# Kernel tuning notes

Measured on AMD Instinct MI355X. Metric: run time of the kernel, lower is better.

## Reference

```python
import jax, jax.numpy as jnp
import numpy as np

N_PHI = 64
NK = 16
NS = 8
B = 512
BN_EPS = 1e-3  # keras BatchNormalization default
LRELU_ALPHA = 0.1


def _cplx(re, im):
    return jax.lax.complex(re, im)


def _conjT(x):
    return jnp.conj(jnp.swapaxes(x, -1, -2))


def setup_inputs() -> dict:
    key = jax.random.key(0)
    ks = jax.random.split(key, 10)

    def cn(k, shape, scale=1.0):
        kr, ki = jax.random.split(k)
        return scale * _cplx(jax.random.normal(kr, shape, jnp.float32),
                             jax.random.normal(ki, shape, jnp.float32))

    # Phi: unit-modulus RIS phase matrix [B, 64, 64]
    theta = jax.random.uniform(ks[0], (B, N_PHI, N_PHI), jnp.float32, 0.0, 2.0 * np.pi)
    Phi = _cplx(jnp.cos(theta), jnp.sin(theta))

    # G_hat_k^H : [Nk, B, 64, Ns]
    G_h = cn(ks[1], (NK, B, N_PHI, NS), 1.0 / np.sqrt(N_PHI))

    # Lam_k: Hermitian PSD + I -> invertible, [Nk, B, Ns, Ns]
    A = cn(ks[2], (NK, B, NS, NS), 0.3)
    Lam = A @ _conjT(A) + jnp.eye(NS, dtype=jnp.complex64)

    # C_k: Hermitian PSD + eps*I, [Nk, B, 64, 64]
    D = cn(ks[3], (NK, B, N_PHI, N_PHI), 0.1)
    C = D @ _conjT(D) + 0.1 * jnp.eye(N_PHI, dtype=jnp.complex64)

    Beta = jax.random.uniform(ks[4], (NK, B, 1, 1), jnp.float32, 0.5, 1.5)

    return {
        "Phi_re": jnp.real(Phi), "Phi_im": jnp.imag(Phi),
        "G_h_re": jnp.real(G_h), "G_h_im": jnp.imag(G_h),
        "Lam_re": jnp.real(Lam), "Lam_im": jnp.imag(Lam),
        "C_re": jnp.real(C), "C_im": jnp.imag(C),
        "Beta": Beta,
        "bn_gamma": jnp.ones((2 * N_PHI,), jnp.float32),
        "bn_beta": jnp.zeros((2 * N_PHI,), jnp.float32),
        "bn_mean": 0.1 * jax.random.normal(ks[5], (2 * N_PHI,), jnp.float32),
        "bn_var": jax.random.uniform(ks[6], (2 * N_PHI,), jnp.float32, 0.5, 1.5),
        "w": 0.1 * jax.random.normal(ks[7], (2 * N_PHI, 1), jnp.float32),
        "b": jnp.zeros((1,), jnp.float32),
    }


def _forward(Phi_re, Phi_im, G_h_re, G_h_im, Lam_re, Lam_im, C_re, C_im, Beta,
             bn_gamma, bn_beta, bn_mean, bn_var, w, b):
    Phi = _cplx(Phi_re, Phi_im)            # [B, 64, 64]
    G_h = _cplx(G_h_re, G_h_im)            # [Nk, B, 64, Ns]
    Lam = _cplx(Lam_re, Lam_im)            # [Nk, B, Ns, Ns]
    C = _cplx(C_re, C_im)                  # [Nk, B, 64, 64]
    Beta_c = _cplx(Beta, jnp.zeros_like(Beta))

    # --- learned step size: Phi @ ones(64,1) == row sums -> BN -> Dense(leaky_relu) ---
    Phi_p_vec = jnp.sum(Phi, axis=2)                                   # [B, 64]
    iq = jnp.concatenate([jnp.real(Phi_p_vec), jnp.imag(Phi_p_vec)], axis=1)  # [B, 128]
    t = bn_gamma * (iq - bn_mean) * jax.lax.rsqrt(bn_var + BN_EPS) + bn_beta
    s = t @ w + b                                                      # [B, 1]
    step = jnp.where(s >= 0, s, LRELU_ALPHA * s)

    # --- batched per-user Euclidean gradient (replaces python loop over Nk) ---
    G = _conjT(G_h)                                                    # [Nk, B, Ns, 64]
    M = jnp.einsum('kbse,bef->kbsf', G, Phi)                           # G_k @ Phi
    T = jnp.einsum('kbsf,kbfg->kbsg', M, C)                            # G_k Phi C_k
    Q = jnp.linalg.inv(Lam) + T @ _conjT(M) / Beta_c                   # [Nk, B, Ns, Ns]
    Qi = jnp.linalg.inv(Q)
    Qi2 = Qi @ Qi
    eg_k = jnp.einsum('kbfs,kbst,kbtg->kbfg', G_h, Qi2, T) / Beta_c    # [Nk, B, 64, 64]
    eg = -(jnp.sum(eg_k, axis=0) / NK) * jnp.eye(N_PHI, dtype=jnp.complex64)

    # --- Riemannian gradient / projection step ---
    proj = jnp.real(eg * jnp.conj(Phi))
    rg = eg - _cplx(proj, jnp.zeros_like(proj)) * Phi
    nrm = jnp.sqrt(jnp.sum(jnp.abs(rg) ** 2, axis=(1, 2), keepdims=True))  # fro norm [B,1,1]
    nrm_c = _cplx(nrm, jnp.zeros_like(nrm))
    step_c = _cplx(step, jnp.zeros_like(step))[:, :, None]             # [B, 1, 1]
    Phi_new = Phi - step_c * rg / nrm_c

    # --- magnitude constraint |Phi| <= 1 ---
    ab = jnp.abs(Phi_new)
    den = jnp.maximum(ab - 1.0, 0.0) + 1.0
    return Phi_new / _cplx(den, jnp.zeros_like(den))


def reference(Phi_re, Phi_im, G_h_re, G_h_im, Lam_re, Lam_im, C_re, C_im, Beta,
              bn_gamma, bn_beta, bn_mean, bn_var, w, b):
    return _forward(Phi_re, Phi_im, G_h_re, G_h_im, Lam_re, Lam_im, C_re, C_im,
                    Beta, bn_gamma, bn_beta, bn_mean, bn_var, w, b)
```

## Files before the change

### kernel.cpp

```cpp
#include <hip/hip_runtime.h>

#define NPHI 64
#define NS 8
#define NK 16
#define BATCH 512

typedef __attribute__((__ext_vector_type__(2))) float v2f;

#define PK_BL(acc, p, b)  asm("v_pk_fma_f32 %0, %1, %2, %0 op_sel:[0,0,0] op_sel_hi:[1,0,1]" : "+v"(acc) : "v"(p), "v"(b))
#define PK_BH(acc, p, b)  asm("v_pk_fma_f32 %0, %1, %2, %0 op_sel:[0,1,0] op_sel_hi:[1,1,1]" : "+v"(acc) : "v"(p), "v"(b))
#define PK_BLN(acc, p, b) asm("v_pk_fma_f32 %0, %1, %2, %0 op_sel:[0,0,0] op_sel_hi:[1,0,1] neg_lo:[0,1,0] neg_hi:[0,1,0]" : "+v"(acc) : "v"(p), "v"(b))
#define PK_X(acc, p, b)   asm("v_pk_fma_f32 %0, %1, %2, %0 op_sel:[1,1,0] op_sel_hi:[0,1,1] neg_lo:[1,0,0]" : "+v"(acc) : "v"(p), "v"(b))
#define PK_XH(acc, p, b)  asm("v_pk_fma_f32 %0, %1, %2, %0 op_sel:[1,1,0] op_sel_hi:[0,1,1] neg_hi:[1,0,0]" : "+v"(acc) : "v"(p), "v"(b))
#define PK_XLO(acc, p, b) asm("v_pk_fma_f32 %0, %1, %2, %0 op_sel:[1,0,0] op_sel_hi:[0,0,1] neg_hi:[1,0,0]" : "+v"(acc) : "v"(p), "v"(b))

__device__ __forceinline__ void cinv8(float& ar, float& ai, int lane) {
    const int i = lane >> 3, j = lane & 7;
#pragma unroll
    for (int p = 0; p < 8; ++p) {
        const float pr = __shfl(ar, p * 9, 64);
        const float pi = __shfl(ai, p * 9, 64);
        const float den = pr * pr + pi * pi;
        const float rr = pr / den, ri = -pi / den;
        const float aipr = __shfl(ar, (i << 3) | p, 64);
        const float aipi = __shfl(ai, (i << 3) | p, 64);
        const float apjr = __shfl(ar, (p << 3) | j, 64);
        const float apji = __shfl(ai, (p << 3) | j, 64);
        const float br = rr * apjr - ri * apji;
        const float bi = rr * apji + ri * apjr;
        const float er = ar - (aipr * br - aipi * bi);
        const float ei = ai - (aipr * bi + aipi * br);
        const float rowr = rr * ar - ri * ai;
        const float rowi = rr * ai + ri * ar;
        const bool ip = (i == p), jp = (j == p);
        const float nr = ip ? (jp ? rr : rowr) : (jp ? -rowr : er);
        const float ni = ip ? (jp ? ri : rowi) : (jp ? -rowi : ei);
        ar = nr; ai = ni;
    }
}

__global__ __launch_bounds__(256, 2) void k_grad_diag(
    const float* __restrict__ PhiR, const float* __restrict__ PhiI,
    const float* __restrict__ GhR, const float* __restrict__ GhI,
    const float* __restrict__ LamR, const float* __restrict__ LamI,
    const float* __restrict__ CR, const float* __restrict__ CI,
    const float* __restrict__ Beta,
    float* __restrict__ out, int region)
{
    const int tid = threadIdx.x;
    const int w = tid >> 6;
    const int lane = tid & 63;
    const int gw = blockIdx.x * 4 + w;
    const int k = gw & (NK - 1);
    const int b = gw >> 4;
    const int kb = k * BATCH + b;

    __shared__ __align__(16) float2 sM[4][NPHI][10];
    __shared__ float2 sQ2[4][64];

    const float* phiR = PhiR + b * 4096;
    const float* phiI = PhiI + b * 4096;
    const float* ghR = GhR + kb * 512;
    const float* ghI = GhI + kb * 512;
    const float invb = 1.0f / Beta[kb];

    v2f accr[4], acci[4];
    v2f acc2[8];

    {
#pragma unroll
        for (int sp = 0; sp < 4; ++sp) { accr[sp] = (v2f)0.f; acci[sp] = (v2f)0.f; }
        float pA[4], qA[4], pB[4], qB[4];
#pragma unroll
        for (int u = 0; u < 4; ++u) {
            pA[u] = phiR[u * 64 + lane];
            qA[u] = phiI[u * 64 + lane];
        }
#pragma unroll 1
        for (int eb = 0; eb < 64; eb += 8) {
#pragma unroll
            for (int u = 0; u < 4; ++u) {
                pB[u] = phiR[(eb + 4 + u) * 64 + lane];
                qB[u] = phiI[(eb + 4 + u) * 64 + lane];
            }
#pragma unroll
            for (int u = 0; u < 4; ++u) {
                const int e = eb + u;
                const v2f* g2 = (const v2f*)(ghR + e * 8);
                const v2f* h2 = (const v2f*)(ghI + e * 8);
                v2f pp; pp.x = pA[u]; pp.y = qA[u];
#pragma unroll
                for (int sp = 0; sp < 4; ++sp) {
                    const v2f g = g2[sp];
                    const v2f h = h2[sp];
                    PK_BL(accr[sp], g, pp);
                    PK_BH(accr[sp], h, pp);
                    PK_BH(acci[sp], g, pp);
                    PK_BLN(acci[sp], h, pp);
                }
            }
            if (eb + 8 < 64) {
#pragma unroll
                for (int u = 0; u < 4; ++u) {
                    pA[u] = phiR[(eb + 8 + u) * 64 + lane];
                    qA[u] = phiI[(eb + 8 + u) * 64 + lane];
                }
            }
#pragma unroll
            for (int u = 0; u < 4; ++u) {
                const int e = eb + 4 + u;
                const v2f* g2 = (const v2f*)(ghR + e * 8);
                const v2f* h2 = (const v2f*)(ghI + e * 8);
                v2f pp; pp.x = pB[u]; pp.y = qB[u];
#pragma unroll
                for (int sp = 0; sp < 4; ++sp) {
                    const v2f g = g2[sp];
                    const v2f h = h2[sp];
                    PK_BL(accr[sp], g, pp);
                    PK_BH(accr[sp], h, pp);
                    PK_BH(acci[sp], g, pp);
                    PK_BLN(acci[sp], h, pp);
                }
            }
        }
#pragma unroll
        for (int sp = 0; sp < 4; ++sp) {
            sM[w][lane][2 * sp]     = make_float2(accr[sp].x, acci[sp].x);
            sM[w][lane][2 * sp + 1] = make_float2(accr[sp].y, acci[sp].y);
        }
    }

    {
        const float* cR = CR + (size_t)kb * 4096;
        const float* cI = CI + (size_t)kb * 4096;
#pragma unroll
        for (int s = 0; s < 8; ++s) acc2[s] = (v2f)0.f;
        float pA[4], qA[4], pB[4], qB[4];
#pragma unroll
        for (int u = 0; u < 4; ++u) {
            pA[u] = cR[u * 64 + lane];
            qA[u] = cI[u * 64 + lane];
        }
#pragma unroll 1
        for (int fb = 0; fb < 64; fb += 8) {
#pragma unroll
            for (int u = 0; u < 4; ++u) {
                pB[u] = cR[(fb + 4 + u) * 64 + lane];
                qB[u] = cI[(fb + 4 + u) * 64 + lane];
            }
#pragma unroll
            for (int u = 0; u < 4; ++u) {
                const int f = fb + u;
                const v2f* mrow = (const v2f*)(&sM[w][f][0]);
                v2f cc; cc.x = pA[u]; cc.y = qA[u];
#pragma unroll
                for (int s = 0; s < 8; ++s) {
                    const v2f ms = mrow[s];
                    PK_BL(acc2[s], cc, ms);
                    PK_X(acc2[s], cc, ms);
                }
            }
            if (fb + 8 < 64) {
#pragma unroll
                for (int u = 0; u < 4; ++u) {
                    pA[u] = cR[(fb + 8 + u) * 64 + lane];
                    qA[u] = cI[(fb + 8 + u) * 64 + lane];
                }
            }
#pragma unroll
            for (int u = 0; u < 4; ++u) {
                const int f = fb + 4 + u;
                const v2f* mrow = (const v2f*)(&sM[w][f][0]);
                v2f cc; cc.x = pB[u]; cc.y = qB[u];
#pragma unroll
                for (int s = 0; s < 8; ++s) {
                    const v2f ms = mrow[s];
                    PK_BL(acc2[s], cc, ms);
                    PK_X(acc2[s], cc, ms);
                }
            }
        }
    }

    float sre, sim;
    {
        const bool l0 = (lane & 1) != 0;
        const bool l1 = (lane & 2) != 0;
        const bool l2 = (lane & 4) != 0;
        v2f Sv = (v2f)0.f;
#pragma unroll
        for (int s = 0; s < 8; ++s) {
            v2f p[8];
#pragma unroll
            for (int t = 0; t < 8; ++t) {
                v2f acc = (v2f)0.f;
                const v2f mre = accr[t >> 1];
                const v2f mim = acci[t >> 1];
                if (t & 1) { PK_BH(acc, acc2[s], mre); PK_XH(acc, acc2[s], mim); }
                else       { PK_BL(acc, acc2[s], mre); PK_XLO(acc, acc2[s], mim); }
                p[t] = acc;
            }
            v2f q[4];
#pragma unroll
            for (int j = 0; j < 4; ++j) {
                v2f snd = l0 ? p[2 * j] : p[2 * j + 1];
                v2f kp  = l0 ? p[2 * j + 1] : p[2 * j];
                kp.x += __shfl_xor(snd.x, 1, 64);
                kp.y += __shfl_xor(snd.y, 1, 64);
                q[j] = kp;
            }
            v2f r[2];
#pragma unroll
            for (int m = 0; m < 2; ++m) {
                v2f snd = l1 ? q[2 * m] : q[2 * m + 1];
                v2f kp  = l1 ? q[2 * m + 1] : q[2 * m];
                kp.x += __shfl_xor(snd.x, 2, 64);
                kp.y += __shfl_xor(snd.y, 2, 64);
                r[m] = kp;
            }
            v2f snd = l2 ? r[0] : r[1];
            v2f v   = l2 ? r[1] : r[0];
            v.x += __shfl_xor(snd.x, 4, 64);
            v.y += __shfl_xor(snd.y, 4, 64);
            v.x += __shfl_xor(v.x, 8, 64);  v.y += __shfl_xor(v.y, 8, 64);
            v.x += __shfl_xor(v.x, 16, 64); v.y += __shfl_xor(v.y, 16, 64);
            v.x += __shfl_xor(v.x, 32, 64); v.y += __shfl_xor(v.y, 32, 64);
            Sv = ((lane >> 3) == s) ? v : Sv;
        }
        sre = Sv.x * invb; sim = Sv.y * invb;
    }

    {
        float ar = LamR[kb * 64 + lane];
        float ai = LamI[kb * 64 + lane];
        cinv8(ar, ai, lane);
        ar += sre; ai += sim;
        cinv8(ar, ai, lane);
        const int i = lane >> 3, j = lane & 7;
        float qr = 0.f, qi = 0.f;
#pragma unroll
        for (int t = 0; t < 8; ++t) {
            const float xr = __shfl(ar, (i << 3) | t, 64);
            const float xi = __shfl(ai, (i << 3) | t, 64);
            const float yr = __shfl(ar, (t << 3) | j, 64);
            const float yi = __shfl(ai, (t << 3) | j, 64);
            qr += xr * yr - xi * yi;
            qi += xr * yi + xi * yr;
        }
        sQ2[w][lane] = make_float2(qr, qi);
    }

    {
        const float4 a0 = *(const float4*)(ghR + lane * 8);
        const float4 a1 = *(const float4*)(ghR + lane * 8 + 4);
        const float4 c0 = *(const float4*)(ghI + lane * 8);
        const float4 c1 = *(const float4*)(ghI + lane * 8 + 4);
        const float gfr[8] = {a0.x, a0.y, a0.z, a0.w, a1.x, a1.y, a1.z, a1.w};
        const float gfi[8] = {c0.x, c0.y, c0.z, c0.w, c1.x, c1.y, c1.z, c1.w};
        float dre = 0.f, dim = 0.f;
#pragma unroll
        for (int s = 0; s < 8; ++s) {
            float yr = 0.f, yi = 0.f;
#pragma unroll
            for (int t = 0; t < 8; ++t) {
                const float2 q = sQ2[w][s * 8 + t];
                yr += q.x * acc2[t].x - q.y * acc2[t].y;
                yi += q.x * acc2[t].y + q.y * acc2[t].x;
            }
            dre += gfr[s] * yr - gfi[s] * yi;
            dim += gfr[s] * yi + gfi[s] * yr;
        }
        float2* scr = (float2*)(out + (size_t)b * region + k * 128);
        scr[lane] = make_float2(dre * invb, dim * invb);
    }
}

__global__ __launch_bounds__(256) void k_finalize(
    const float* __restrict__ PhiR, const float* __restrict__ PhiI,
    const float* __restrict__ bnG, const float* __restrict__ bnB,
    const float* __restrict__ bnM, const float* __restrict__ bnV,
    const float* __restrict__ W, const float* __restrict__ Bb,
    float* __restrict__ out, int region, int cplx)
{
    const int b = blockIdx.x;
    const int tid = threadIdx.x;
    __shared__ float sIQ[128];
    __shared__ float sRed[2];
    __shared__ float sDre[64], sDim[64];

    const float* phiR = PhiR + b * 4096;
    const float* phiI = PhiI + b * 4096;
    float* outp = out + (size_t)b * region;

    float er = 0.f, ei = 0.f;
    if (tid < 64) {
        const int f = tid;
#pragma unroll
        for (int kk = 0; kk < NK; ++kk) {
            const float2 dv = ((const float2*)(outp + kk * 128))[f];
            er += dv.x; ei += dv.y;
        }
    }

    {
        const int r = tid >> 2, pq = tid & 3;
        float sr = 0.f, si = 0.f;
        const float4* a4 = (const float4*)(phiR + r * 64 + pq * 16);
        const float4* c4 = (const float4*)(phiI + r * 64 + pq * 16);
#pragma unroll
        for (int q = 0; q < 4; ++q) {
            const float4 a = a4[q]; sr += (a.x + a.y) + (a.z + a.w);
            const float4 c = c4[q]; si += (c.x + c.y) + (c.z + c.w);
        }
        sr += __shfl_xor(sr, 1, 64); si += __shfl_xor(si, 1, 64);
        sr += __shfl_xor(sr, 2, 64); si += __shfl_xor(si, 2, 64);
        if (pq == 0) { sIQ[r] = sr; sIQ[64 + r] = si; }
    }
    __syncthreads();

    if (tid < 128) {
        const float v = sIQ[tid];
        const float t = bnG[tid] * (v - bnM[tid]) * rsqrtf(bnV[tid] + 1e-3f) + bnB[tid];
        float contrib = t * W[tid];
#pragma unroll
        for (int o = 1; o < 64; o <<= 1) contrib += __shfl_xor(contrib, o, 64);
        if ((tid & 63) == 0) sRed[tid >> 6] = contrib;
    }
    __syncthreads();
    const float s_lin = sRed[0] + sRed[1] + Bb[0];
    const float step = (s_lin >= 0.f) ? s_lin : 0.1f * s_lin;

    if (tid < 64) {
        const int f = tid;
        er *= -(1.0f / NK); ei *= -(1.0f / NK);
        const float prr = phiR[f * 65];
        const float pii = phiI[f * 65];
        const float proj = er * prr + ei * pii;
        const float rr = er - proj * prr;
        const float ri = ei - proj * pii;
        float n2 = rr * rr + ri * ri;
#pragma unroll
        for (int o = 1; o < 64; o <<= 1) n2 += __shfl_xor(n2, o, 64);
        const float sc = step / sqrtf(n2);
        sDre[f] = sc * rr;
        sDim[f] = sc * ri;
    }
    __syncthreads();

#pragma unroll
    for (int p = 0; p < 4; ++p) {
        const int base = p * 1024 + tid * 4;
        const float4 a = *(const float4*)(phiR + base);
        const float4 c = *(const float4*)(phiI + base);
        const int row = base >> 6;
        const int col0 = base & 63;
        float re[4] = {a.x, a.y, a.z, a.w};
        float im[4] = {c.x, c.y, c.z, c.w};
#pragma unroll
        for (int q = 0; q < 4; ++q) {
            if (row == col0 + q) { re[q] -= sDre[row]; im[q] -= sDim[row]; }
            const float ab = sqrtf(re[q] * re[q] + im[q] * im[q]);
            const float den = fmaxf(ab - 1.f, 0.f) + 1.f;
            re[q] /= den; im[q] /= den;
        }
        if (cplx) {
            *(float4*)(outp + base * 2)     = make_float4(re[0], im[0], re[1], im[1]);
            *(float4*)(outp + base * 2 + 4) = make_float4(re[2], im[2], re[3], im[3]);
        } else {
            *(float4*)(outp + base) = make_float4(re[0], re[1], re[2], re[3]);
        }
    }
}

extern "C" void kernel_launch(void* const* d_in, const int* in_sizes, int n_in,
                              void* d_out, int out_size, void* d_ws, size_t ws_size,
                              hipStream_t stream) {
    const float* PhiR = (const float*)d_in[0];
    const float* PhiI = (const float*)d_in[1];
    const float* GhR  = (const float*)d_in[2];
    const float* GhI  = (const float*)d_in[3];
    const float* LamR = (const float*)d_in[4];
    const float* LamI = (const float*)d_in[5];
    const float* CR   = (const float*)d_in[6];
    const float* CI   = (const float*)d_in[7];
    const float* Beta = (const float*)d_in[8];
    const float* bnG  = (const float*)d_in[9];
    const float* bnB  = (const float*)d_in[10];
    const float* bnM  = (const float*)d_in[11];
    const float* bnV  = (const float*)d_in[12];
    const float* W    = (const float*)d_in[13];
    const float* Bb   = (const float*)d_in[14];
    float* outp = (float*)d_out;

    const int cplx = (out_size >= 3000000) ? 1 : 0;
    const int region = cplx ? 8192 : 4096;

    k_grad_diag<<<(NK * BATCH) / 4, 256, 0, stream>>>(PhiR, PhiI, GhR, GhI,
                                                      LamR, LamI, CR, CI, Beta,
                                                      outp, region);
    k_finalize<<<BATCH, 256, 0, stream>>>(PhiR, PhiI,
                                          bnG, bnB, bnM, bnV, W, Bb,
                                          outp, region, cplx);
}
```

Measured before the change: 138.5 us.

## Process two k-slices per wavefront to reuse Phi loads and interleave work

Each wavefront now handles two users (k pairs) for the same batch element, so the Phi column loads in the first matmul are shared across two G_h products. The C-matrix stage, the 8x8 complex inversions and the shuffle reductions are interleaved for both users to expose more independent instructions and hide latency. The grid is halved accordingly. This roughly doubles register and LDS use per wave, which risks spills or lower occupancy under the existing launch bounds.

Result: slower. 164.1 us (+18.5%).

```diff
diff --git a/kernel.cpp b/kernel.cpp
--- a/kernel.cpp
+++ b/kernel.cpp
@@ -14,28 +14,50 @@
 #define PK_XH(acc, p, b)  asm("v_pk_fma_f32 %0, %1, %2, %0 op_sel:[1,1,0] op_sel_hi:[0,1,1] neg_hi:[1,0,0]" : "+v"(acc) : "v"(p), "v"(b))
 #define PK_XLO(acc, p, b) asm("v_pk_fma_f32 %0, %1, %2, %0 op_sel:[1,0,0] op_sel_hi:[0,0,1] neg_hi:[1,0,0]" : "+v"(acc) : "v"(p), "v"(b))
 
-__device__ __forceinline__ void cinv8(float& ar, float& ai, int lane) {
+__device__ __forceinline__ void cinv8_pair(float& ar0, float& ai0,
+                                           float& ar1, float& ai1, int lane) {
     const int i = lane >> 3, j = lane & 7;
 #pragma unroll
     for (int p = 0; p < 8; ++p) {
-        const float pr = __shfl(ar, p * 9, 64);
-        const float pi = __shfl(ai, p * 9, 64);
-        const float den = pr * pr + pi * pi;
-        const float rr = pr / den, ri = -pi / den;
-        const float aipr = __shfl(ar, (i << 3) | p, 64);
-        const float aipi = __shfl(ai, (i << 3) | p, 64);
-        const float apjr = __shfl(ar, (p << 3) | j, 64);
-        const float apji = __shfl(ai, (p << 3) | j, 64);
-        const float br = rr * apjr - ri * apji;
-        const float bi = rr * apji + ri * apjr;
-        const float er = ar - (aipr * br - aipi * bi);
-        const float ei = ai - (aipr * bi + aipi * br);
-        const float rowr = rr * ar - ri * ai;
-        const float rowi = rr * ai + ri * ar;
+        const float pr0 = __shfl(ar0, p * 9, 64);
+        const float pi0 = __shfl(ai0, p * 9, 64);
+        const float pr1 = __shfl(ar1, p * 9, 64);
+        const float pi1 = __shfl(ai1, p * 9, 64);
+        const float aipr0 = __shfl(ar0, (i << 3) | p, 64);
+        const float aipi0 = __shfl(ai0, (i << 3) | p, 64);
+        const float aipr1 = __shfl(ar1, (i << 3) | p, 64);
+        const float aipi1 = __shfl(ai1, (i << 3) | p, 64);
+        const float apjr0 = __shfl(ar0, (p << 3) | j, 64);
+        const float apji0 = __shfl(ai0, (p << 3) | j, 64);
+        const float apjr1 = __shfl(ar1, (p << 3) | j, 64);
+        const float apji1 = __shfl(ai1, (p << 3) | j, 64);
         const bool ip = (i == p), jp = (j == p);
-        const float nr = ip ? (jp ? rr : rowr) : (jp ? -rowr : er);
-        const float ni = ip ? (jp ? ri : rowi) : (jp ? -rowi : ei);
-        ar = nr; ai = ni;
+        {
+            const float den = pr0 * pr0 + pi0 * pi0;
+            const float rr = pr0 / den, ri = -pi0 / den;
+            const float br = rr * apjr0 - ri * apji0;
+            const float bi = rr * apji0 + ri * apjr0;
+            const float er = ar0 - (aipr0 * br - aipi0 * bi);
+            const float ei = ai0 - (aipr0 * bi + aipi0 * br);
+            const float rowr = rr * ar0 - ri * ai0;
+            const float rowi = rr * ai0 + ri * ar0;
+            const float nr = ip ? (jp ? rr : rowr) : (jp ? -rowr : er);
+            const float ni = ip ? (jp ? ri : rowi) : (jp ? -rowi : ei);
+            ar0 = nr; ai0 = ni;
+        }
+        {
+            const float den = pr1 * pr1 + pi1 * pi1;
+            const float rr = pr1 / den, ri = -pi1 / den;
+            const float br = rr * apjr1 - ri * apji1;
+            const float bi = rr * apji1 + ri * apjr1;
+            const float er = ar1 - (aipr1 * br - aipi1 * bi);
+            const float ei = ai1 - (aipr1 * bi + aipi1 * br);
+            const float rowr = rr * ar1 - ri * ai1;
+            const float rowi = rr * ai1 + ri * ar1;
+            const float nr = ip ? (jp ? rr : rowr) : (jp ? -rowr : er);
+            const float ni = ip ? (jp ? ri : rowi) : (jp ? -rowi : ei);
+            ar1 = nr; ai1 = ni;
+        }
     }
 }
 
@@ -51,25 +73,33 @@
     const int w = tid >> 6;
     const int lane = tid & 63;
     const int gw = blockIdx.x * 4 + w;
-    const int k = gw & (NK - 1);
-    const int b = gw >> 4;
-    const int kb = k * BATCH + b;
-
-    __shared__ __align__(16) float2 sM[4][NPHI][10];
-    __shared__ float2 sQ2[4][64];
+    const int b = gw >> 3;
+    const int kp = gw & 7;
+    const int k0 = kp * 2, k1 = kp * 2 + 1;
+    const int kb0 = k0 * BATCH + b;
+    const int kb1 = k1 * BATCH + b;
+
+    __shared__ float2 sM[4][2][NPHI][9];
+    __shared__ float2 sQ2[4][2][64];
 
     const float* phiR = PhiR + b * 4096;
     const float* phiI = PhiI + b * 4096;
-    const float* ghR = GhR + kb * 512;
-    const float* ghI = GhI + kb * 512;
-    const float invb = 1.0f / Beta[kb];
-
-    v2f accr[4], acci[4];
-    v2f acc2[8];
+    const float* ghR0 = GhR + kb0 * 512;
+    const float* ghI0 = GhI + kb0 * 512;
+    const float* ghR1 = GhR + kb1 * 512;
+    const float* ghI1 = GhI + kb1 * 512;
+    const float invb0 = 1.0f / Beta[kb0];
+    const float invb1 = 1.0f / Beta[kb1];
+
+    v2f a0r[4], a0i[4], a1r[4], a1i[4];
+    v2f t0[8], t1[8];
 
     {
 #pragma unroll
-        for (int sp = 0; sp < 4; ++sp) { accr[sp] = (v2f)0.f; acci[sp] = (v2f)0.f; }
+        for (int sp = 0; sp < 4; ++sp) {
+            a0r[sp] = (v2f)0.f; a0i[sp] = (v2f)0.f;
+            a1r[sp] = (v2f)0.f; a1i[sp] = (v2f)0.f;
+        }
         float pA[4], qA[4], pB[4], qB[4];
 #pragma unroll
         for (int u = 0; u < 4; ++u) {
@@ -86,17 +116,19 @@
 #pragma unroll
             for (int u = 0; u < 4; ++u) {
                 const int e = eb + u;
-                const v2f* g2 = (const v2f*)(ghR + e * 8);
-                const v2f* h2 = (const v2f*)(ghI + e * 8);
+                const v2f* g20 = (const v2f*)(ghR0 + e * 8);
+                const v2f* h20 = (const v2f*)(ghI0 + e * 8);
+                const v2f* g21 = (const v2f*)(ghR1 + e * 8);
+                const v2f* h21 = (const v2f*)(ghI1 + e * 8);
                 v2f pp; pp.x = pA[u]; pp.y = qA[u];
 #pragma unroll
                 for (int sp = 0; sp < 4; ++sp) {
-                    const v2f g = g2[sp];
-                    const v2f h = h2[sp];
-                    PK_BL(accr[sp], g, pp);
-                    PK_BH(accr[sp], h, pp);
-                    PK_BH(acci[sp], g, pp);
-                    PK_BLN(acci[sp], h, pp);
+                    const v2f g0 = g20[sp], h0 = h20[sp];
+                    PK_BL(a0r[sp], g0, pp);  PK_BH(a0r[sp], h0, pp);
+                    PK_BH(a0i[sp], g0, pp);  PK_BLN(a0i[sp], h0, pp);
+                    const v2f g1 = g21[sp], h1 = h21[sp];
+                    PK_BL(a1r[sp], g1, pp);  PK_BH(a1r[sp], h1, pp);
+                    PK_BH(a1i[sp], g1, pp);  PK_BLN(a1i[sp], h1, pp);
                 }
             }
             if (eb + 8 < 64) {
@@ -109,152 +141,198 @@
 #pragma unroll
             for (int u = 0; u < 4; ++u) {
                 const int e = eb + 4 + u;
-                const v2f* g2 = (const v2f*)(ghR + e * 8);
-                const v2f* h2 = (const v2f*)(ghI + e * 8);
+                const v2f* g20 = (const v2f*)(ghR0 + e * 8);
+                const v2f* h20 = (const v2f*)(ghI0 + e * 8);
+                const v2f* g21 = (const v2f*)(ghR1 + e * 8);
+                const v2f* h21 = (const v2f*)(ghI1 + e * 8);
                 v2f pp; pp.x = pB[u]; pp.y = qB[u];
 #pragma unroll
                 for (int sp = 0; sp < 4; ++sp) {
-                    const v2f g = g2[sp];
-                    const v2f h = h2[sp];
-                    PK_BL(accr[sp], g, pp);
-                    PK_BH(accr[sp], h, pp);
-                    PK_BH(acci[sp], g, pp);
-                    PK_BLN(acci[sp], h, pp);
+                    const v2f g0 = g20[sp], h0 = h20[sp];
+                    PK_BL(a0r[sp], g0, pp);  PK_BH(a0r[sp], h0, pp);
+                    PK_BH(a0i[sp], g0, pp);  PK_BLN(a0i[sp], h0, pp);
+                    const v2f g1 = g21[sp], h1 = h21[sp];
+                    PK_BL(a1r[sp], g1, pp);  PK_BH(a1r[sp], h1, pp);
+                    PK_BH(a1i[sp], g1, pp);  PK_BLN(a1i[sp], h1, pp);
                 }
             }
         }
 #pragma unroll
         for (int sp = 0; sp < 4; ++sp) {
-            sM[w][lane][2 * sp]     = make_float2(accr[sp].x, acci[sp].x);
-            sM[w][lane][2 * sp + 1] = make_float2(accr[sp].y, acci[sp].y);
+            sM[w][0][lane][2 * sp]     = make_float2(a0r[sp].x, a0i[sp].x);
+            sM[w][0][lane][2 * sp + 1] = make_float2(a0r[sp].y, a0i[sp].y);
+            sM[w][1][lane][2 * sp]     = make_float2(a1r[sp].x, a1i[sp].x);
+            sM[w][1][lane][2 * sp + 1] = make_float2(a1r[sp].y, a1i[sp].y);
         }
     }
 
     {
-        const float* cR = CR + (size_t)kb * 4096;
-        const float* cI = CI + (size_t)kb * 4096;
-#pragma unroll
-        for (int s = 0; s < 8; ++s) acc2[s] = (v2f)0.f;
-        float pA[4], qA[4], pB[4], qB[4];
-#pragma unroll
-        for (int u = 0; u < 4; ++u) {
-            pA[u] = cR[u * 64 + lane];
-            qA[u] = cI[u * 64 + lane];
+        const float* cR0 = CR + (size_t)kb0 * 4096;
+        const float* cI0 = CI + (size_t)kb0 * 4096;
+        const float* cR1 = CR + (size_t)kb1 * 4096;
+        const float* cI1 = CI + (size_t)kb1 * 4096;
+#pragma unroll
+        for (int s = 0; s < 8; ++s) { t0[s] = (v2f)0.f; t1[s] = (v2f)0.f; }
+        float c0A[2], d0A[2], c1A[2], d1A[2];
+        float c0B[2], d0B[2], c1B[2], d1B[2];
+#pragma unroll
+        for (int u = 0; u < 2; ++u) {
+            c0A[u] = cR0[u * 64 + lane];  d0A[u] = cI0[u * 64 + lane];
+            c1A[u] = cR1[u * 64 + lane];  d1A[u] = cI1[u * 64 + lane];
         }
 #pragma unroll 1
-        for (int fb = 0; fb < 64; fb += 8) {
-#pragma unroll
-            for (int u = 0; u < 4; ++u) {
-                pB[u] = cR[(fb + 4 + u) * 64 + lane];
-                qB[u] = cI[(fb + 4 + u) * 64 + lane];
-            }
-#pragma unroll
-            for (int u = 0; u < 4; ++u) {
+        for (int fb = 0; fb < 64; fb += 4) {
+#pragma unroll
+            for (int u = 0; u < 2; ++u) {
+                c0B[u] = cR0[(fb + 2 + u) * 64 + lane];  d0B[u] = cI0[(fb + 2 + u) * 64 + lane];
+                c1B[u] = cR1[(fb + 2 + u) * 64 + lane];  d1B[u] = cI1[(fb + 2 + u) * 64 + lane];
+            }
+#pragma unroll
+            for (int u = 0; u < 2; ++u) {
                 const int f = fb + u;
-                const v2f* mrow = (const v2f*)(&sM[w][f][0]);
-                v2f cc; cc.x = pA[u]; cc.y = qA[u];
+                const v2f* m0 = (const v2f*)(&sM[w][0][f][0]);
+                const v2f* m1 = (const v2f*)(&sM[w][1][f][0]);
+                v2f cc0; cc0.x = c0A[u]; cc0.y = d0A[u];
+                v2f cc1; cc1.x = c1A[u]; cc1.y = d1A[u];
 #pragma unroll
                 for (int s = 0; s < 8; ++s) {
-                    const v2f ms = mrow[s];
-                    PK_BL(acc2[s], cc, ms);
-                    PK_X(acc2[s], cc, ms);
+                    const v2f ms0 = m0[s];
+                    PK_BL(t0[s], cc0, ms0);  PK_X(t0[s], cc0, ms0);
+                    const v2f ms1 = m1[s];
+                    PK_BL(t1[s], cc1, ms1);  PK_X(t1[s], cc1, ms1);
                 }
             }
-            if (fb + 8 < 64) {
-#pragma unroll
-                for (int u = 0; u < 4; ++u) {
-                    pA[u] = cR[(fb + 8 + u) * 64 + lane];
-                    qA[u] = cI[(fb + 8 + u) * 64 + lane];
+            if (fb + 4 < 64) {
+#pragma unroll
+                for (int u = 0; u < 2; ++u) {
+                    c0A[u] = cR0[(fb + 4 + u) * 64 + lane];  d0A[u] = cI0[(fb + 4 + u) * 64 + lane];
+                    c1A[u] = cR1[(fb + 4 + u) * 64 + lane];  d1A[u] = cI1[(fb + 4 + u) * 64 + lane];
                 }
             }
 #pragma unroll
-            for (int u = 0; u < 4; ++u) {
-                const int f = fb + 4 + u;
-                const v2f* mrow = (const v2f*)(&sM[w][f][0]);
-                v2f cc; cc.x = pB[u]; cc.y = qB[u];
+            for (int u = 0; u < 2; ++u) {
+                const int f = fb + 2 + u;
+                const v2f* m0 = (const v2f*)(&sM[w][0][f][0]);
+                const v2f* m1 = (const v2f*)(&sM[w][1][f][0]);
+                v2f cc0; cc0.x = c0B[u]; cc0.y = d0B[u];
+                v2f cc1; cc1.x = c1B[u]; cc1.y = d1B[u];
 #pragma unroll
                 for (int s = 0; s < 8; ++s) {
-                    const v2f ms = mrow[s];
-                    PK_BL(acc2[s], cc, ms);
-                    PK_X(acc2[s], cc, ms);
+                    const v2f ms0 = m0[s];
+                    PK_BL(t0[s], cc0, ms0);  PK_X(t0[s], cc0, ms0);
+                    const v2f ms1 = m1[s];
+                    PK_BL(t1[s], cc1, ms1);  PK_X(t1[s], cc1, ms1);
                 }
             }
         }
     }
 
-    float sre, sim;
+    const float lr0 = LamR[kb0 * 64 + lane], li0 = LamI[kb0 * 64 + lane];
+    const float lr1 = LamR[kb1 * 64 + lane], li1 = LamI[kb1 * 64 + lane];
+
+    float sre0, sim0, sre1, sim1;
     {
         const bool l0 = (lane & 1) != 0;
         const bool l1 = (lane & 2) != 0;
         const bool l2 = (lane & 4) != 0;
-        v2f Sv = (v2f)0.f;
+        v2f Sv0 = (v2f)0.f, Sv1 = (v2f)0.f;
 #pragma unroll
         for (int s = 0; s < 8; ++s) {
-            v2f p[8];
+            v2f p0[8], p1[8];
 #pragma unroll
             for (int t = 0; t < 8; ++t) {
                 v2f acc = (v2f)0.f;
-                const v2f mre = accr[t >> 1];
-                const v2f mim = acci[t >> 1];
-                if (t & 1) { PK_BH(acc, acc2[s], mre); PK_XH(acc, acc2[s], mim); }
-                else       { PK_BL(acc, acc2[s], mre); PK_XLO(acc, acc2[s], mim); }
-                p[t] = acc;
-            }
-            v2f q[4];
+                const v2f mre = a0r[t >> 1], mim = a0i[t >> 1];
+                if (t & 1) { PK_BH(acc, t0[s], mre); PK_XH(acc, t0[s], mim); }
+                else       { PK_BL(acc, t0[s], mre); PK_XLO(acc, t0[s], mim); }
+                p0[t] = acc;
+                v2f acd = (v2f)0.f;
+                const v2f nre = a1r[t >> 1], nim = a1i[t >> 1];
+                if (t & 1) { PK_BH(acd, t1[s], nre); PK_XH(acd, t1[s], nim); }
+                else       { PK_BL(acd, t1[s], nre); PK_XLO(acd, t1[s], nim); }
+                p1[t] = acd;
+            }
+            v2f q0[4], q1[4];
 #pragma unroll
             for (int j = 0; j < 4; ++j) {
-                v2f snd = l0 ? p[2 * j] : p[2 * j + 1];
-                v2f kp  = l0 ? p[2 * j + 1] : p[2 * j];
+                v2f snd = l0 ? p0[2 * j] : p0[2 * j + 1];
+                v2f kp  = l0 ? p0[2 * j + 1] : p0[2 * j];
                 kp.x += __shfl_xor(snd.x, 1, 64);
                 kp.y += __shfl_xor(snd.y, 1, 64);
-                q[j] = kp;
-            }
-            v2f r[2];
+                q0[j] = kp;
+                v2f snd1 = l0 ? p1[2 * j] : p1[2 * j + 1];
+                v2f kp1  = l0 ? p1[2 * j + 1] : p1[2 * j];
+                kp1.x += __shfl_xor(snd1.x, 1, 64);
+                kp1.y += __shfl_xor(snd1.y, 1, 64);
+                q1[j] = kp1;
+            }
+            v2f r0[2], r1[2];
 #pragma unroll
             for (int m = 0; m < 2; ++m) {
-                v2f snd = l1 ? q[2 * m] : q[2 * m + 1];
-                v2f kp  = l1 ? q[2 * m + 1] : q[2 * m];
+                v2f snd = l1 ? q0[2 * m] : q0[2 * m + 1];
+                v2f kp  = l1 ? q0[2 * m + 1] : q0[2 * m];
                 kp.x += __shfl_xor(snd.x, 2, 64);
                 kp.y += __shfl_xor(snd.y, 2, 64);
-                r[m] = kp;
-            }
-            v2f snd = l2 ? r[0] : r[1];
-            v2f v   = l2 ? r[1] : r[0];
-            v.x += __shfl_xor(snd.x, 4, 64);
-            v.y += __shfl_xor(snd.y, 4, 64);
-            v.x += __shfl_xor(v.x, 8, 64);  v.y += __shfl_xor(v.y, 8, 64);
-            v.x += __shfl_xor(v.x, 16, 64); v.y += __shfl_xor(v.y, 16, 64);
-            v.x += __shfl_xor(v.x, 32, 64); v.y += __shfl_xor(v.y, 32, 64);
-            Sv = ((lane >> 3) == s) ? v : Sv;
-        }
-        sre = Sv.x * invb; sim = Sv.y * invb;
+                r0[m] = kp;
+                v2f snd1 = l1 ? q1[2 * m] : q1[2 * m + 1];
+                v2f kp1  = l1 ? q1[2 * m + 1] : q1[2 * m];
+                kp1.x += __shfl_xor(snd1.x, 2, 64);
+                kp1.y += __shfl_xor(snd1.y, 2, 64);
+                r1[m] = kp1;
+            }
+            v2f s0 = l2 ? r0[0] : r0[1];
+            v2f v0 = l2 ? r0[1] : r0[0];
+            v0.x += __shfl_xor(s0.x, 4, 64);
+            v0.y += __shfl_xor(s0.y, 4, 64);
+            v2f s1 = l2 ? r1[0] : r1[1];
+            v2f v1 = l2 ? r1[1] : r1[0];
+            v1.x += __shfl_xor(s1.x, 4, 64);
+            v1.y += __shfl_xor(s1.y, 4, 64);
+            v0.x += __shfl_xor(v0.x, 8, 64);  v0.y += __shfl_xor(v0.y, 8, 64);
+            v1.x += __shfl_xor(v1.x, 8, 64);  v1.y += __shfl_xor(v1.y, 8, 64);
+            v0.x += __shfl_xor(v0.x, 16, 64); v0.y += __shfl_xor(v0.y, 16, 64);
+            v1.x += __shfl_xor(v1.x, 16, 64); v1.y += __shfl_xor(v1.y, 16, 64);
+            v0.x += __shfl_xor(v0.x, 32, 64); v0.y += __shfl_xor(v0.y, 32, 64);
+            v1.x += __shfl_xor(v1.x, 32, 64); v1.y += __shfl_xor(v1.y, 32, 64);
+            Sv0 = ((lane >> 3) == s) ? v0 : Sv0;
+            Sv1 = ((lane >> 3) == s) ? v1 : Sv1;
+        }
+        sre0 = Sv0.x * invb0; sim0 = Sv0.y * invb0;
+        sre1 = Sv1.x * invb1; sim1 = Sv1.y * invb1;
     }
 
     {
-        float ar = LamR[kb * 64 + lane];
-        float ai = LamI[kb * 64 + lane];
-        cinv8(ar, ai, lane);
-        ar += sre; ai += sim;
-        cinv8(ar, ai, lane);
+        float ar0 = lr0, ai0 = li0, ar1 = lr1, ai1 = li1;
+        cinv8_pair(ar0, ai0, ar1, ai1, lane);
+        ar0 += sre0; ai0 += sim0;
+        ar1 += sre1; ai1 += sim1;
+        cinv8_pair(ar0, ai0, ar1, ai1, lane);
         const int i = lane >> 3, j = lane & 7;
-        float qr = 0.f, qi = 0.f;
+        float q0r = 0.f, q0i = 0.f, q1r = 0.f, q1i = 0.f;
 #pragma unroll
         for (int t = 0; t < 8; ++t) {
-            const float xr = __shfl(ar, (i << 3) | t, 64);
-            const float xi = __shfl(ai, (i << 3) | t, 64);
-            const float yr = __shfl(ar, (t << 3) | j, 64);
-            const float yi = __shfl(ai, (t << 3) | j, 64);
-            qr += xr * yr - xi * yi;
-            qi += xr * yi + xi * yr;
-        }
-        sQ2[w][lane] = make_float2(qr, qi);
+            const float x0r = __shfl(ar0, (i << 3) | t, 64);
+            const float x0i = __shfl(ai0, (i << 3) | t, 64);
+            const float y0r = __shfl(ar0, (t << 3) | j, 64);
+            const float y0i = __shfl(ai0, (t << 3) | j, 64);
+            const float x1r = __shfl(ar1, (i << 3) | t, 64);
+            const float x1i = __shfl(ai1, (i << 3) | t, 64);
+            const float y1r = __shfl(ar1, (t << 3) | j, 64);
+            const float y1i = __shfl(ai1, (t << 3) | j, 64);
+            q0r += x0r * y0r - x0i * y0i;
+            q0i += x0r * y0i + x0i * y0r;
+            q1r += x1r * y1r - x1i * y1i;
+            q1i += x1r * y1i + x1i * y1r;
+        }
+        sQ2[w][0][lane] = make_float2(q0r, q0i);
+        sQ2[w][1][lane] = make_float2(q1r, q1i);
     }
 
     {
-        const float4 a0 = *(const float4*)(ghR + lane * 8);
-        const float4 a1 = *(const float4*)(ghR + lane * 8 + 4);
-        const float4 c0 = *(const float4*)(ghI + lane * 8);
-        const float4 c1 = *(const float4*)(ghI + lane * 8 + 4);
+        const float4 a0 = *(const float4*)(ghR0 + lane * 8);
+        const float4 a1 = *(const float4*)(ghR0 + lane * 8 + 4);
+        const float4 c0 = *(const float4*)(ghI0 + lane * 8);
+        const float4 c1 = *(const float4*)(ghI0 + lane * 8 + 4);
         const float gfr[8] = {a0.x, a0.y, a0.z, a0.w, a1.x, a1.y, a1.z, a1.w};
         const float gfi[8] = {c0.x, c0.y, c0.z, c0.w, c1.x, c1.y, c1.z, c1.w};
         float dre = 0.f, dim = 0.f;
@@ -263,15 +341,37 @@
             float yr = 0.f, yi = 0.f;
 #pragma unroll
             for (int t = 0; t < 8; ++t) {
-                const float2 q = sQ2[w][s * 8 + t];
-                yr += q.x * acc2[t].x - q.y * acc2[t].y;
-                yi += q.x * acc2[t].y + q.y * acc2[t].x;
+                const float2 q = sQ2[w][0][s * 8 + t];
+                yr += q.x * t0[t].x - q.y * t0[t].y;
+                yi += q.x * t0[t].y + q.y * t0[t].x;
             }
             dre += gfr[s] * yr - gfi[s] * yi;
             dim += gfr[s] * yi + gfi[s] * yr;
         }
-        float2* scr = (float2*)(out + (size_t)b * region + k * 128);
-        scr[lane] = make_float2(dre * invb, dim * invb);
+        float2* scr0 = (float2*)(out + (size_t)b * region + k0 * 128);
+        scr0[lane] = make_float2(dre * invb0, dim * invb0);
+
+        const float4 e0 = *(const float4*)(ghR1 + lane * 8);
+        const float4 e1 = *(const float4*)(ghR1 + lane * 8 + 4);
+        const float4 f0 = *(const float4*)(ghI1 + lane * 8);
+        const float4 f1 = *(const float4*)(ghI1 + lane * 8 + 4);
+        const float hfr[8] = {e0.x, e0.y, e0.z, e0.w, e1.x, e1.y, e1.z, e1.w};
+        const float hfi[8] = {f0.x, f0.y, f0.z, f0.w, f1.x, f1.y, f1.z, f1.w};
+        float er = 0.f, ei = 0.f;
+#pragma unroll
+        for (int s = 0; s < 8; ++s) {
+            float yr = 0.f, yi = 0.f;
+#pragma unroll
+            for (int t = 0; t < 8; ++t) {
+                const float2 q = sQ2[w][1][s * 8 + t];
+                yr += q.x * t1[t].x - q.y * t1[t].y;
+                yi += q.x * t1[t].y + q.y * t1[t].x;
+            }
+            er += hfr[s] * yr - hfi[s] * yi;
+            ei += hfr[s] * yi + hfi[s] * yr;
+        }
+        float2* scr1 = (float2*)(out + (size_t)b * region + k1 * 128);
+        scr1[lane] = make_float2(er * invb1, ei * invb1);
     }
 }
 
@@ -395,7 +495,7 @@
     const int cplx = (out_size >= 3000000) ? 1 : 0;
     const int region = cplx ? 8192 : 4096;
 
-    k_grad_diag<<<(NK * BATCH) / 4, 256, 0, stream>>>(PhiR, PhiI, GhR, GhI,
+    k_grad_diag<<<(NK * BATCH) / 8, 256, 0, stream>>>(PhiR, PhiI, GhR, GhI,
                                                       LamR, LamI, CR, CI, Beta,
                                                       outp, region);
     k_finalize<<<BATCH, 256, 0, stream>>>(PhiR, PhiI,
```
